# Kernel tuning notes

Measured on AMD Instinct MI355X. Metric: run time of the kernel, lower is better.

The kernel has to match this reference:

```python
import jax, jax.numpy as jnp
import numpy as np

B, N, C = 16, 4096, 91            # images, proposals/image, classes (incl. background)
H, W = 800.0, 1333.0              # image shape
SCORE_THRESH = 0.05
NMS_THRESH = 0.5
K = 100                           # detections_per_img (greedy NMS steps)
M = 4096                          # top-M candidate prefilter before NMS
OFFSET = 1.0e4                    # class offset for batched NMS (>> max coord)
DW_CLAMP = float(np.log(1000.0 / 16.0))


def setup_inputs():
    key = jax.random.key(0)
    k1, k2, k3, k4, k5, k6 = jax.random.split(key, 6)
    class_logits = jax.random.normal(k1, (B * N, C), jnp.float32) * 2.0
    box_regression = jax.random.normal(k2, (B * N, C * 4), jnp.float32) * 0.1
    # valid proposal boxes (x1 < x2, y1 < y2, inside image)
    x1 = jax.random.uniform(k3, (B, N, 1)) * (W - 64.0)
    y1 = jax.random.uniform(k4, (B, N, 1)) * (H - 64.0)
    bw = jax.random.uniform(k5, (B, N, 1)) * 256.0 + 16.0
    bh = jax.random.uniform(k6, (B, N, 1)) * 256.0 + 16.0
    proposals = jnp.concatenate([x1, y1, jnp.minimum(x1 + bw, W), jnp.minimum(y1 + bh, H)], -1)
    return {"class_logits": class_logits, "box_regression": box_regression, "proposals": proposals}


def _decode_and_clip(rel, props):
    w = props[..., 2] - props[..., 0]
    h = props[..., 3] - props[..., 1]
    cx = props[..., 0] + 0.5 * w
    cy = props[..., 1] + 0.5 * h
    dx = rel[..., 0] / 10.0
    dy = rel[..., 1] / 10.0
    dw = jnp.minimum(rel[..., 2] / 5.0, DW_CLAMP)
    dh = jnp.minimum(rel[..., 3] / 5.0, DW_CLAMP)
    pcx = dx * w[..., None] + cx[..., None]
    pcy = dy * h[..., None] + cy[..., None]
    pw = jnp.exp(dw) * w[..., None]
    ph = jnp.exp(dh) * h[..., None]
    boxes = jnp.stack([
        jnp.clip(pcx - 0.5 * pw, 0.0, W),
        jnp.clip(pcy - 0.5 * ph, 0.0, H),
        jnp.clip(pcx + 0.5 * pw, 0.0, W),
        jnp.clip(pcy + 0.5 * ph, 0.0, H)], -1)  # [B,N,C,4]
    return boxes


def _greedy_nms(boxes, scores):
    # boxes: [M,4] (already class-offset), scores: [M] (suppressed entries == -1)
    x1, y1, x2, y2 = boxes[:, 0], boxes[:, 1], boxes[:, 2], boxes[:, 3]
    area = (x2 - x1) * (y2 - y1)

    def step(sc, _):
        i = jnp.argmax(sc)
        s = sc[i]
        valid = s > 0.0
        iw = jnp.clip(jnp.minimum(x2, x2[i]) - jnp.maximum(x1, x1[i]), 0.0)
        ih = jnp.clip(jnp.minimum(y2, y2[i]) - jnp.maximum(y1, y1[i]), 0.0)
        inter = iw * ih
        iou = inter / (area + area[i] - inter + 1e-9)
        sc = jnp.where((iou > NMS_THRESH) & valid, -1.0, sc)
        sc = sc.at[i].set(-1.0)
        return sc, (i, s, valid)

    _, (idx, ss, vv) = jax.lax.scan(step, scores, None, length=K)
    return idx, ss, vv


def _post_image(boxes_all, scores_all):
    # boxes_all: [N,C,4] decoded+clipped, scores_all: [N,C] softmax scores
    boxes = boxes_all[:, 1:, :].reshape(-1, 4)          # drop background class 0
    scores = scores_all[:, 1:].reshape(-1)              # [N*(C-1)], class fastest
    labels = jnp.tile(jnp.arange(1, C, dtype=jnp.int32), N)
    scores = jnp.where(scores > SCORE_THRESH, scores, -1.0)
    top_s, top_i = jax.lax.top_k(scores, M)
    b = boxes[top_i]
    l = labels[top_i]
    ob = b + (l.astype(jnp.float32) * OFFSET)[:, None]  # batched_nms class-offset trick
    idx, ss, vv = _greedy_nms(ob, top_s)
    out_boxes = jnp.where(vv[:, None], b[idx], 0.0)     # [K,4]
    out_scores = jnp.where(vv, ss, 0.0)                 # [K]
    out_labels = jnp.where(vv, l[idx], -1)              # [K]
    return out_boxes, out_scores, out_labels, vv


def reference(class_logits, box_regression, proposals):
    pred_scores = jax.nn.softmax(class_logits, -1).reshape(B, N, C)
    rel = box_regression.reshape(B, N, C, 4)
    pred_boxes = _decode_and_clip(rel, proposals)
    boxes, scores, labels, valid = jax.vmap(_post_image)(pred_boxes, pred_scores)
    return boxes, scores, labels, valid
```

## Files before the change

kernel.cpp:

```cpp
#include <hip/hip_runtime.h>

typedef unsigned long long u64;
typedef unsigned int u32;

#define BDIM 16
#define NP   4096
#define NC   91
#define NCM1 90
#define MSEL 4096
#define NSORT 1024
#define KOUT 100
#define RSLOT 19
#define CAP_D (NP * RSLOT)
#define SCORE_T 0.05f
#define NMS_T   0.5f
#define OFFSETF 10000.0f
#define DW_CLAMP_F 4.135166556742356f
#define WF 1333.0f
#define HF 800.0f
#define GTMIN 384

#define TN 1024
#define RPB 64

#define DECODE_BODY(kvar, bvar, BOXDST, PACKDST)                                   \
    {                                                                              \
        int flat = (int)(~(u32)(kvar));                                            \
        int nidx = flat / NCM1;                                                    \
        int c    = flat - nidx * NCM1 + 1;                                         \
        const float* pr = props + ((long)(bvar) * NP + nidx) * 4;                  \
        float x1 = pr[0], y1 = pr[1], x2 = pr[2], y2 = pr[3];                      \
        float w = x2 - x1, h = y2 - y1;                                            \
        float cx = x1 + 0.5f * w, cy = y1 + 0.5f * h;                              \
        const float* rr = boxreg + (((long)(bvar) * NP + nidx) * NC + c) * 4;      \
        float dx = rr[0] / 10.0f, dy = rr[1] / 10.0f;                              \
        float dw = fminf(rr[2] / 5.0f, DW_CLAMP_F);                                \
        float dh = fminf(rr[3] / 5.0f, DW_CLAMP_F);                                \
        float pcx = __fadd_rn(__fmul_rn(dx, w), cx);                               \
        float pcy = __fadd_rn(__fmul_rn(dy, h), cy);                               \
        float pw  = __fmul_rn(expf(dw), w);                                        \
        float ph2 = __fmul_rn(expf(dh), h);                                        \
        float bx1 = fminf(fmaxf(pcx - 0.5f * pw, 0.0f), WF);                       \
        float by1 = fminf(fmaxf(pcy - 0.5f * ph2, 0.0f), HF);                      \
        float bx2 = fminf(fmaxf(pcx + 0.5f * pw, 0.0f), WF);                       \
        float by2 = fminf(fmaxf(pcy + 0.5f * ph2, 0.0f), HF);                      \
        BOXDST = make_float4(bx1, by1, bx2, by2);                                  \
        float offB = (float)c * OFFSETF;                                           \
        float ox1 = bx1 + offB, oy1 = by1 + offB;                                  \
        float ox2 = bx2 + offB, oy2 = by2 + offB;                                  \
        PACKDST = make_float2((ox2 - ox1) * (oy2 - oy1), (float)c);                \
    }

__global__ __launch_bounds__(64) void k_zero(int* __restrict__ gcount) {
    if (threadIdx.x < BDIM) gcount[threadIdx.x] = 0;
}

__global__ __launch_bounds__(256) void k_soft(const float* __restrict__ logits,
                                              u64* __restrict__ dense,
                                              int* __restrict__ gcount) {
    __shared__ u64 stage[RPB * RSLOT];
    __shared__ int s_cnt, s_base;

    int blk  = blockIdx.x;
    int b    = blk >> 6;
    int lane = threadIdx.x & 63;
    int wid  = threadIdx.x >> 6;

    if (threadIdx.x == 0) s_cnt = 0;
    __syncthreads();

    u64 lm = (1ull << lane) - 1ull;
    for (int it = 0; it < RPB / 4; ++it) {
        int row = blk * RPB + it * 4 + wid;
        const float* lg = logits + (long)row * NC;

        float v0 = lg[lane];
        float v1 = (lane < NC - 64) ? lg[64 + lane] : -3.0e38f;
        float mx = fmaxf(v0, v1);
#pragma unroll
        for (int s = 32; s; s >>= 1) mx = fmaxf(mx, __shfl_xor(mx, s));
        float e0 = expf(v0 - mx);
        float e1 = (lane < NC - 64) ? expf(v1 - mx) : 0.0f;
        float sum = e0 + e1;
#pragma unroll
        for (int s = 32; s; s >>= 1) sum += __shfl_xor(sum, s);

        float s0 = e0 / sum;
        float s1 = e1 / sum;

        int n = row & (NP - 1);
        bool p0 = (lane >= 1) && (s0 > SCORE_T);
        bool p1 = (lane < NC - 64) && (s1 > SCORE_T);
        u64 m0 = __ballot(p0);
        u64 m1 = __ballot(p1);
        int c0  = __popcll(m0);
        int cnt = c0 + __popcll(m1);

        int base = 0;
        if (lane == 0 && cnt) base = atomicAdd(&s_cnt, cnt);
        base = __shfl(base, 0);
        if (p0) {
            int pos  = base + __popcll(m0 & lm);
            int flat = n * NCM1 + (lane - 1);
            stage[pos] = ((u64)__float_as_uint(s0) << 32) | (u32)(~(u32)flat);
        }
        if (p1) {
            int pos  = base + c0 + __popcll(m1 & lm);
            int flat = n * NCM1 + (64 + lane - 1);
            stage[pos] = ((u64)__float_as_uint(s1) << 32) | (u32)(~(u32)flat);
        }
    }
    __syncthreads();

    if (threadIdx.x == 0) s_base = atomicAdd(&gcount[b], s_cnt);
    __syncthreads();
    int m = s_cnt, base = s_base;
    u64* kb = dense + (long)b * CAP_D + base;
    for (int i = threadIdx.x; i < m; i += 256) kb[i] = stage[i];
}

__device__ __forceinline__ u64 radix_rank(const u64* __restrict__ kb, int n, int rank,
                                          int* hist, int* p_sel, int* p_gt, int tid) {
    u64 prefix = 0, mask = 0;
    const int shifts[6] = {53, 42, 31, 20, 10, 0};
    const int bitsv [6] = {11, 11, 11, 11, 10, 10};

    for (int pass = 0; pass < 6; ++pass) {
        int shift = shifts[pass];
        int nb = 1 << bitsv[pass];
        if (tid < nb) hist[tid] = 0;
        if (tid + 1024 < nb) hist[tid + 1024] = 0;
        __syncthreads();
        for (int i = tid; i < n; i += 1024) {
            u64 k = kb[i];
            if ((k & mask) == prefix)
                atomicAdd(&hist[(int)((k >> shift) & (u64)(nb - 1))], 1);
        }
        __syncthreads();
        for (int d = 1; d < nb; d <<= 1) {
            int v0 = 0, v1 = 0;
            if (tid < nb && tid + d < nb) v0 = hist[tid + d];
            if (tid + 1024 < nb && tid + 1024 + d < nb) v1 = hist[tid + 1024 + d];
            __syncthreads();
            if (tid < nb) hist[tid] += v0;
            if (tid + 1024 < nb) hist[tid + 1024] += v1;
            __syncthreads();
        }
        for (int j = tid; j < nb; j += 1024) {
            int c  = hist[j];
            int cn = (j + 1 < nb) ? hist[j + 1] : 0;
            if (c >= rank && cn < rank) { *p_sel = j; *p_gt = cn; }
        }
        __syncthreads();
        prefix |= ((u64)(*p_sel)) << shift;
        mask   |= ((u64)(nb - 1)) << shift;
        rank   -= *p_gt;
        __syncthreads();
    }
    return prefix;
}

__device__ __forceinline__ u64 radix_upper(const u64* __restrict__ kb, int n, int rank,
                                           int* hist, int* p_sel, int* p_gt, int tid) {
    int rank0 = rank;
    u64 prefix = 0, mask = 0;
    const int shifts[6] = {53, 42, 31, 20, 10, 0};
    const int bitsv [6] = {11, 11, 11, 11, 10, 10};

    for (int pass = 0; pass < 6; ++pass) {
        int shift = shifts[pass];
        int nb = 1 << bitsv[pass];
        if (tid < nb) hist[tid] = 0;
        if (tid + 1024 < nb) hist[tid + 1024] = 0;
        __syncthreads();
        for (int i = tid; i < n; i += 1024) {
            u64 k = kb[i];
            if ((k & mask) == prefix)
                atomicAdd(&hist[(int)((k >> shift) & (u64)(nb - 1))], 1);
        }
        __syncthreads();
        for (int d = 1; d < nb; d <<= 1) {
            int v0 = 0, v1 = 0;
            if (tid < nb && tid + d < nb) v0 = hist[tid + d];
            if (tid + 1024 < nb && tid + 1024 + d < nb) v1 = hist[tid + 1024 + d];
            __syncthreads();
            if (tid < nb) hist[tid] += v0;
            if (tid + 1024 < nb) hist[tid + 1024] += v1;
            __syncthreads();
        }
        for (int j = tid; j < nb; j += 1024) {
            int c  = hist[j];
            int cn = (j + 1 < nb) ? hist[j + 1] : 0;
            if (c >= rank && cn < rank) { *p_sel = j; *p_gt = cn; }
        }
        __syncthreads();
        int sel = *p_sel, gt = *p_gt;
        rank -= gt;
        __syncthreads();
        if (pass < 5) {
            if (rank0 - rank >= GTMIN)
                return prefix + ((u64)(sel + 1) << shift);
            prefix |= ((u64)sel) << shift;
            mask   |= ((u64)(nb - 1)) << shift;
        } else {
            prefix |= ((u64)sel) << shift;
        }
    }
    return prefix;
}

__global__ __launch_bounds__(TN) void k_post(const u64* __restrict__ dense,
                                             const int* __restrict__ gcount,
                                             const float* __restrict__ boxreg,
                                             const float* __restrict__ props,
                                             float* __restrict__ out) {
    __shared__ __align__(16) char ldsbuf[131072];
    __shared__ int s_cnt, s_nacc, s_sel, s_gt;

    float4* sbox  = (float4*)ldsbuf;
    float2* spack = (float2*)(ldsbuf + 16384);
    u64*    skey  = (u64*)(ldsbuf + 24576);
    int*    hist  = (int*)(ldsbuf + 32768);

    int b = blockIdx.x, tid = threadIdx.x;
    int lane = tid & 63, wid = tid >> 6;
    int n = gcount[b]; if (n > CAP_D) n = CAP_D;
    const u64* kb = dense + (long)b * CAP_D;
    u64 lm = (1ull << lane) - 1ull;
    int npad = (n + TN - 1) & ~(TN - 1);

    u64 Bthr = 0ull;
    if (n > NSORT) Bthr = radix_upper(kb, n, NSORT, hist, &s_sel, &s_gt, tid);

    skey[tid] = 0ull;
    if (tid == 0) s_cnt = 0;
    __syncthreads();
    for (int i0 = tid; i0 < npad; i0 += TN) {
        bool inb = (i0 < n);
        u64 k = inb ? kb[i0] : 0ull;
        bool pred = inb && (k >= Bthr);
        u64 mb_ = __ballot(pred);
        int cnt = __popcll(mb_);
        int bp = 0;
        if (lane == 0 && cnt) bp = atomicAdd(&s_cnt, cnt);
        bp = __shfl(bp, 0);
        if (pred) {
            int pos = bp + __popcll(mb_ & lm);
            if (pos < NSORT) skey[pos] = k;
        }
    }
    __syncthreads();
    int mb = s_cnt; if (mb > NSORT) mb = NSORT;

    {
        u64 r = skey[tid];
        for (int kk = 2; kk <= NSORT; kk <<= 1) {
            for (int j = kk >> 1; j; j >>= 1) {
                u64 p;
                if (j >= 64) {
                    skey[tid] = r;
                    __syncthreads();
                    p = skey[tid ^ j];
                    __syncthreads();
                } else {
                    p = __shfl_xor(r, j);
                }
                bool lower = (tid & j) == 0;
                bool desc  = ((tid & kk) == 0);
                u64 mx = (r > p) ? r : p;
                u64 mn = (r > p) ? p : r;
                r = (lower == desc) ? mx : mn;
            }
        }
        skey[tid] = r;
        __syncthreads();
    }

    for (int i = tid; i < mb; i += TN) {
        u64 k = skey[i];
        float4 bx; float2 pk;
        DECODE_BODY(k, b, bx, pk);
        sbox[i] = bx;
        spack[i] = pk;
    }
    __syncthreads();

    float ax1_0 = 0, ay1_0 = 0, ax2_0 = 0, ay2_0 = 0, aar_0 = 0;
    float ax1_1 = 0, ay1_1 = 0, ax2_1 = 0, ay2_1 = 0, aar_1 = 0;
    int alb_0 = -1, alb_1 = -1;
    u64 aky_0 = 0, aky_1 = 0;
    int nacc = 0;

    if (wid == 0) {
        float4 Bv = sbox[0];
        float2 pk = spack[0];
        u64    ck = skey[0];
        for (int i = 0; i < mb && nacc < KOUT; ++i) {
            int ip = (i + 1 < mb) ? i + 1 : i;
            float4 nBv = sbox[ip];
            float2 npk = spack[ip];
            u64    nck = skey[ip];

            float areaB = pk.x;
            float labf  = pk.y;
            float off   = __fmul_rn(labf, OFFSETF);
            bool conf = false;
            if (lane < nacc && (float)alb_0 == labf) {
                float op1x = __fadd_rn(fminf(ax2_0, Bv.z), off);
                float op2x = __fadd_rn(fmaxf(ax1_0, Bv.x), off);
                float iw = fmaxf(op1x - op2x, 0.0f);
                float op1y = __fadd_rn(fminf(ay2_0, Bv.w), off);
                float op2y = __fadd_rn(fmaxf(ay1_0, Bv.y), off);
                float ih = fmaxf(op1y - op2y, 0.0f);
                float inter = iw * ih;
                float denom = areaB + aar_0 - inter + 1e-9f;
                if (inter / denom > NMS_T) conf = true;
            }
            if (64 + lane < nacc && (float)alb_1 == labf) {
                float op1x = __fadd_rn(fminf(ax2_1, Bv.z), off);
                float op2x = __fadd_rn(fmaxf(ax1_1, Bv.x), off);
                float iw = fmaxf(op1x - op2x, 0.0f);
                float op1y = __fadd_rn(fminf(ay2_1, Bv.w), off);
                float op2y = __fadd_rn(fmaxf(ay1_1, Bv.y), off);
                float ih = fmaxf(op1y - op2y, 0.0f);
                float inter = iw * ih;
                float denom = areaB + aar_1 - inter + 1e-9f;
                if (inter / denom > NMS_T) conf = true;
            }
            if (__ballot(conf) == 0ull) {
                if (nacc < 64) {
                    if (lane == nacc) {
                        ax1_0 = Bv.x; ay1_0 = Bv.y; ax2_0 = Bv.z; ay2_0 = Bv.w;
                        aar_0 = areaB; alb_0 = (int)labf; aky_0 = ck;
                    }
                } else {
                    if (lane == nacc - 64) {
                        ax1_1 = Bv.x; ay1_1 = Bv.y; ax2_1 = Bv.z; ay2_1 = Bv.w;
                        aar_1 = areaB; alb_1 = (int)labf; aky_1 = ck;
                    }
                }
                ++nacc;
            }
            Bv = nBv; pk = npk; ck = nck;
        }
        if (lane == 0) s_nacc = nacc;
    }
    __syncthreads();

    if (s_nacc < KOUT && Bthr != 0ull) {
        u64 T = 0ull;
        if (n > MSEL) T = radix_rank(kb, n, MSEL, hist, &s_sel, &s_gt, tid);

        u64*    fkey  = (u64*)ldsbuf;
        float4* fbox  = (float4*)(ldsbuf + 32768);
        float2* fpack = (float2*)(ldsbuf + 98304);

        for (int i = tid; i < MSEL; i += TN) fkey[i] = 0ull;
        if (tid == 0) s_cnt = 0;
        __syncthreads();
        for (int i0 = tid; i0 < npad; i0 += TN) {
            bool inb = (i0 < n);
            u64 k = inb ? kb[i0] : 0ull;
            bool pred = inb && (k >= T && k < Bthr);
            u64 mb_ = __ballot(pred);
            int cnt = __popcll(mb_);
            int bp = 0;
            if (lane == 0 && cnt) bp = atomicAdd(&s_cnt, cnt);
            bp = __shfl(bp, 0);
            if (pred) {
                int pos = bp + __popcll(mb_ & lm);
                if (pos < MSEL) fkey[pos] = k;
            }
        }
        __syncthreads();
        int mb2 = s_cnt; if (mb2 > MSEL) mb2 = MSEL;

        for (int kk = 2; kk <= MSEL; kk <<= 1) {
            for (int j = kk >> 1; j > 0; j >>= 1) {
                for (int t = tid; t < MSEL; t += TN) {
                    int l = t ^ j;
                    if (l > t) {
                        u64 a = fkey[t], c = fkey[l];
                        bool up = ((t & kk) == 0);
                        bool sw = up ? (a < c) : (a > c);
                        if (sw) { fkey[t] = c; fkey[l] = a; }
                    }
                }
                __syncthreads();
            }
        }

        for (int i = tid; i < mb2; i += TN) {
            u64 k = fkey[i];
            float4 bx; float2 pk;
            DECODE_BODY(k, b, bx, pk);
            fbox[i] = bx;
            fpack[i] = pk;
        }
        __syncthreads();

        if (wid == 0) {
            float4 Bv = fbox[0];
            float2 pk = fpack[0];
            u64    ck = fkey[0];
            for (int i = 0; i < mb2 && nacc < KOUT; ++i) {
                int ip = (i + 1 < mb2) ? i + 1 : i;
                float4 nBv = fbox[ip];
                float2 npk = fpack[ip];
                u64    nck = fkey[ip];

                float areaB = pk.x;
                float labf  = pk.y;
                float off   = __fmul_rn(labf, OFFSETF);
                bool conf = false;
                if (lane < nacc && (float)alb_0 == labf) {
                    float op1x = __fadd_rn(fminf(ax2_0, Bv.z), off);
                    float op2x = __fadd_rn(fmaxf(ax1_0, Bv.x), off);
                    float iw = fmaxf(op1x - op2x, 0.0f);
                    float op1y = __fadd_rn(fminf(ay2_0, Bv.w), off);
                    float op2y = __fadd_rn(fmaxf(ay1_0, Bv.y), off);
                    float ih = fmaxf(op1y - op2y, 0.0f);
                    float inter = iw * ih;
                    float denom = areaB + aar_0 - inter + 1e-9f;
                    if (inter / denom > NMS_T) conf = true;
                }
                if (64 + lane < nacc && (float)alb_1 == labf) {
                    float op1x = __fadd_rn(fminf(ax2_1, Bv.z), off);
                    float op2x = __fadd_rn(fmaxf(ax1_1, Bv.x), off);
                    float iw = fmaxf(op1x - op2x, 0.0f);
                    float op1y = __fadd_rn(fminf(ay2_1, Bv.w), off);
                    float op2y = __fadd_rn(fmaxf(ay1_1, Bv.y), off);
                    float ih = fmaxf(op1y - op2y, 0.0f);
                    float inter = iw * ih;
                    float denom = areaB + aar_1 - inter + 1e-9f;
                    if (inter / denom > NMS_T) conf = true;
                }
                if (__ballot(conf) == 0ull) {
                    if (nacc < 64) {
                        if (lane == nacc) {
                            ax1_0 = Bv.x; ay1_0 = Bv.y; ax2_0 = Bv.z; ay2_0 = Bv.w;
                            aar_0 = areaB; alb_0 = (int)labf; aky_0 = ck;
                        }
                    } else {
                        if (lane == nacc - 64) {
                            ax1_1 = Bv.x; ay1_1 = Bv.y; ax2_1 = Bv.z; ay2_1 = Bv.w;
                            aar_1 = areaB; alb_1 = (int)labf; aky_1 = ck;
                        }
                    }
                    ++nacc;
                }
                Bv = nBv; pk = npk; ck = nck;
            }
            if (lane == 0) s_nacc = nacc;
        }
        __syncthreads();
    }

    int na = s_nacc; if (na > KOUT) na = KOUT;
    if (wid == 0) {
        if (lane < na) {
            int a = lane;
            float* ob = out + ((long)b * KOUT + a) * 4;
            ob[0] = ax1_0; ob[1] = ay1_0; ob[2] = ax2_0; ob[3] = ay2_0;
            out[BDIM * KOUT * 4 + b * KOUT + a] = __uint_as_float((u32)(aky_0 >> 32));
            out[BDIM * KOUT * 5 + b * KOUT + a] = (float)alb_0;
            out[BDIM * KOUT * 6 + b * KOUT + a] = 1.0f;
        }
        if (64 + lane < na) {
            int a = 64 + lane;
            float* ob = out + ((long)b * KOUT + a) * 4;
            ob[0] = ax1_1; ob[1] = ay1_1; ob[2] = ax2_1; ob[3] = ay2_1;
            out[BDIM * KOUT * 4 + b * KOUT + a] = __uint_as_float((u32)(aky_1 >> 32));
            out[BDIM * KOUT * 5 + b * KOUT + a] = (float)alb_1;
            out[BDIM * KOUT * 6 + b * KOUT + a] = 1.0f;
        }
    }
    for (int a = tid; a < KOUT; a += TN) {
        if (a >= na) {
            float* ob = out + ((long)b * KOUT + a) * 4;
            ob[0] = 0.0f; ob[1] = 0.0f; ob[2] = 0.0f; ob[3] = 0.0f;
            out[BDIM * KOUT * 4 + b * KOUT + a] = 0.0f;
            out[BDIM * KOUT * 5 + b * KOUT + a] = -1.0f;
            out[BDIM * KOUT * 6 + b * KOUT + a] = 0.0f;
        }
    }
}

extern "C" void kernel_launch(void* const* d_in, const int* in_sizes, int n_in,
                              void* d_out, int out_size, void* d_ws, size_t ws_size,
                              hipStream_t stream) {
    const float* logits = (const float*)d_in[0];
    const float* boxreg = (const float*)d_in[1];
    const float* props  = (const float*)d_in[2];
    float* out = (float*)d_out;

    char* ws = (char*)d_ws;
    int* gcount = (int*)(ws + 0);
    u64* dense  = (u64*)(ws + 1024);

    k_zero<<<1, 64, 0, stream>>>(gcount);
    k_soft<<<(BDIM * NP) / RPB, 256, 0, stream>>>(logits, dense, gcount);
    k_post<<<BDIM, TN, 0, stream>>>(dense, gcount, boxreg, props, out);
}
```

Baseline: 84.18 us.

## Build top-bits histogram and hot-key list in softmax kernel to skip radix passes

The softmax kernel now builds a per-image 2048-bin histogram over the top 11 key bits and also writes a compact list of high-score candidates (score >= 0.25). The post kernel prefix-sums that histogram to find the top-1024 threshold bin directly, so it can usually skip the multi-pass radix select over the dense candidate array. When the threshold lies in the hot range, it compacts from the small hot list instead of rescanning all dense keys. This removes repeated global scans from the single-block-per-image post kernel. In exchange it adds shared atomics and global histogram atomics to k_soft, a larger zeroing kernel, and fallback paths for when the estimate overflows.

```diff
diff --git a/kernel.cpp b/kernel.cpp
--- a/kernel.cpp
+++ b/kernel.cpp
@@ -19,6 +19,8 @@
 #define WF 1333.0f
 #define HF 800.0f
 #define GTMIN 384
+#define HCAP 4096
+#define FKEY (((u64)0x3E800000u) << 32)
 
 #define TN 1024
 #define RPB 64
@@ -51,22 +53,37 @@
         PACKDST = make_float2((ox2 - ox1) * (oy2 - oy1), (float)c);                \
     }
 
-__global__ __launch_bounds__(64) void k_zero(int* __restrict__ gcount) {
-    if (threadIdx.x < BDIM) gcount[threadIdx.x] = 0;
+__global__ __launch_bounds__(1024) void k_zero(int* __restrict__ gcount,
+                                               int* __restrict__ hcnt,
+                                               int* __restrict__ ghist) {
+    int blk = blockIdx.x;
+    if (blk == 0) {
+        if (threadIdx.x < BDIM) gcount[threadIdx.x] = 0;
+        if (threadIdx.x >= 64 && threadIdx.x < 64 + BDIM) hcnt[threadIdx.x - 64] = 0;
+    } else {
+        int* g = ghist + (blk - 1) * 2048;
+        for (int i = threadIdx.x; i < 2048; i += 1024) g[i] = 0;
+    }
 }
 
 __global__ __launch_bounds__(256) void k_soft(const float* __restrict__ logits,
                                               u64* __restrict__ dense,
-                                              int* __restrict__ gcount) {
+                                              int* __restrict__ gcount,
+                                              u64* __restrict__ hot,
+                                              int* __restrict__ hcnt,
+                                              int* __restrict__ ghist) {
     __shared__ u64 stage[RPB * RSLOT];
-    __shared__ int s_cnt, s_base;
+    __shared__ u64 hstage[256];
+    __shared__ int lhist[2048];
+    __shared__ int s_cnt, s_base, s_hcnt, s_hbase;
 
     int blk  = blockIdx.x;
     int b    = blk >> 6;
     int lane = threadIdx.x & 63;
     int wid  = threadIdx.x >> 6;
 
-    if (threadIdx.x == 0) s_cnt = 0;
+    if (threadIdx.x == 0) { s_cnt = 0; s_hcnt = 0; }
+    for (int i = threadIdx.x; i < 2048; i += 256) lhist[i] = 0;
     __syncthreads();
 
     u64 lm = (1ull << lane) - 1ull;
@@ -91,6 +108,8 @@
         int n = row & (NP - 1);
         bool p0 = (lane >= 1) && (s0 > SCORE_T);
         bool p1 = (lane < NC - 64) && (s1 > SCORE_T);
+        u64 key0 = ((u64)__float_as_uint(s0) << 32) | (u32)(~(u32)(n * NCM1 + (lane - 1)));
+        u64 key1 = ((u64)__float_as_uint(s1) << 32) | (u32)(~(u32)(n * NCM1 + (64 + lane - 1)));
         u64 m0 = __ballot(p0);
         u64 m1 = __ballot(p1);
         int c0  = __popcll(m0);
@@ -100,23 +119,46 @@
         if (lane == 0 && cnt) base = atomicAdd(&s_cnt, cnt);
         base = __shfl(base, 0);
         if (p0) {
-            int pos  = base + __popcll(m0 & lm);
-            int flat = n * NCM1 + (lane - 1);
-            stage[pos] = ((u64)__float_as_uint(s0) << 32) | (u32)(~(u32)flat);
+            stage[base + __popcll(m0 & lm)] = key0;
+            atomicAdd(&lhist[(int)(key0 >> 53)], 1);
         }
         if (p1) {
-            int pos  = base + c0 + __popcll(m1 & lm);
-            int flat = n * NCM1 + (64 + lane - 1);
-            stage[pos] = ((u64)__float_as_uint(s1) << 32) | (u32)(~(u32)flat);
-        }
+            stage[base + c0 + __popcll(m1 & lm)] = key1;
+            atomicAdd(&lhist[(int)(key1 >> 53)], 1);
+        }
+
+        bool q0 = p0 && (s0 >= 0.25f);
+        bool q1 = p1 && (s1 >= 0.25f);
+        u64 h0 = __ballot(q0);
+        u64 h1 = __ballot(q1);
+        int hc0 = __popcll(h0);
+        int hrow = hc0 + __popcll(h1);
+        int hb = 0;
+        if (lane == 0 && hrow) hb = atomicAdd(&s_hcnt, hrow);
+        hb = __shfl(hb, 0);
+        if (q0) hstage[hb + __popcll(h0 & lm)] = key0;
+        if (q1) hstage[hb + hc0 + __popcll(h1 & lm)] = key1;
     }
     __syncthreads();
 
-    if (threadIdx.x == 0) s_base = atomicAdd(&gcount[b], s_cnt);
+    if (threadIdx.x == 0) {
+        s_base  = atomicAdd(&gcount[b], s_cnt);
+        s_hbase = atomicAdd(&hcnt[b], s_hcnt);
+    }
     __syncthreads();
     int m = s_cnt, base = s_base;
     u64* kb = dense + (long)b * CAP_D + base;
     for (int i = threadIdx.x; i < m; i += 256) kb[i] = stage[i];
+    int hm = s_hcnt, hb2 = s_hbase;
+    u64* hbp = hot + (long)b * HCAP;
+    for (int i = threadIdx.x; i < hm; i += 256) {
+        int pos = hb2 + i;
+        if (pos < HCAP) hbp[pos] = hstage[i];
+    }
+    for (int i = threadIdx.x; i < 2048; i += 256) {
+        int v = lhist[i];
+        if (v) atomicAdd(&ghist[b * 2048 + i], v);
+    }
 }
 
 __device__ __forceinline__ u64 radix_rank(const u64* __restrict__ kb, int n, int rank,
@@ -211,6 +253,9 @@
 
 __global__ __launch_bounds__(TN) void k_post(const u64* __restrict__ dense,
                                              const int* __restrict__ gcount,
+                                             const u64* __restrict__ hot,
+                                             const int* __restrict__ hcnt,
+                                             const int* __restrict__ ghist,
                                              const float* __restrict__ boxreg,
                                              const float* __restrict__ props,
                                              float* __restrict__ out) {
@@ -230,26 +275,91 @@
     int npad = (n + TN - 1) & ~(TN - 1);
 
     u64 Bthr = 0ull;
-    if (n > NSORT) Bthr = radix_upper(kb, n, NSORT, hist, &s_sel, &s_gt, tid);
+    bool hist_ok = false;
+    if (n > NSORT) {
+        for (int i = tid; i < 2048; i += TN) hist[i] = ghist[b * 2048 + i];
+        __syncthreads();
+        for (int d = 1; d < 2048; d <<= 1) {
+            int v0 = 0, v1 = 0;
+            if (tid + d < 2048) v0 = hist[tid + d];
+            if (tid + 1024 + d < 2048) v1 = hist[tid + 1024 + d];
+            __syncthreads();
+            hist[tid] += v0;
+            if (tid + 1024 + d < 2048 || tid + 1024 < 2048) hist[tid + 1024] += v1;
+            __syncthreads();
+        }
+        for (int j = tid; j < 2048; j += TN) {
+            int c  = hist[j];
+            int cn = (j + 1 < 2048) ? hist[j + 1] : 0;
+            if (c >= NSORT && cn < NSORT) { s_sel = j; s_gt = cn; }
+        }
+        __syncthreads();
+        int sel = s_sel, gt = s_gt;
+        __syncthreads();
+        if (gt >= GTMIN) { Bthr = ((u64)(sel + 1)) << 53; hist_ok = true; }
+        else             Bthr = radix_upper(kb, n, NSORT, hist, &s_sel, &s_gt, tid);
+    }
+    int hn = hcnt[b];
+    bool use_hot = hist_ok && (Bthr >= FKEY) && (hn <= HCAP);
 
     skey[tid] = 0ull;
     if (tid == 0) s_cnt = 0;
     __syncthreads();
-    for (int i0 = tid; i0 < npad; i0 += TN) {
-        bool inb = (i0 < n);
-        u64 k = inb ? kb[i0] : 0ull;
-        bool pred = inb && (k >= Bthr);
-        u64 mb_ = __ballot(pred);
-        int cnt = __popcll(mb_);
-        int bp = 0;
-        if (lane == 0 && cnt) bp = atomicAdd(&s_cnt, cnt);
-        bp = __shfl(bp, 0);
-        if (pred) {
-            int pos = bp + __popcll(mb_ & lm);
-            if (pos < NSORT) skey[pos] = k;
+    if (use_hot) {
+        const u64* hb = hot + (long)b * HCAP;
+        int hpad = (hn + TN - 1) & ~(TN - 1);
+        for (int i0 = tid; i0 < hpad; i0 += TN) {
+            bool inb = (i0 < hn);
+            u64 k = inb ? hb[i0] : 0ull;
+            bool pred = inb && (k >= Bthr);
+            u64 mb_ = __ballot(pred);
+            int cnt = __popcll(mb_);
+            int bp = 0;
+            if (lane == 0 && cnt) bp = atomicAdd(&s_cnt, cnt);
+            bp = __shfl(bp, 0);
+            if (pred) {
+                int pos = bp + __popcll(mb_ & lm);
+                if (pos < NSORT) skey[pos] = k;
+            }
+        }
+    } else {
+        for (int i0 = tid; i0 < npad; i0 += TN) {
+            bool inb = (i0 < n);
+            u64 k = inb ? kb[i0] : 0ull;
+            bool pred = inb && (k >= Bthr);
+            u64 mb_ = __ballot(pred);
+            int cnt = __popcll(mb_);
+            int bp = 0;
+            if (lane == 0 && cnt) bp = atomicAdd(&s_cnt, cnt);
+            bp = __shfl(bp, 0);
+            if (pred) {
+                int pos = bp + __popcll(mb_ & lm);
+                if (pos < NSORT) skey[pos] = k;
+            }
         }
     }
     __syncthreads();
+    if (s_cnt > NSORT) {
+        Bthr = radix_upper(kb, n, NSORT, hist, &s_sel, &s_gt, tid);
+        skey[tid] = 0ull;
+        if (tid == 0) s_cnt = 0;
+        __syncthreads();
+        for (int i0 = tid; i0 < npad; i0 += TN) {
+            bool inb = (i0 < n);
+            u64 k = inb ? kb[i0] : 0ull;
+            bool pred = inb && (k >= Bthr);
+            u64 mb_ = __ballot(pred);
+            int cnt = __popcll(mb_);
+            int bp = 0;
+            if (lane == 0 && cnt) bp = atomicAdd(&s_cnt, cnt);
+            bp = __shfl(bp, 0);
+            if (pred) {
+                int pos = bp + __popcll(mb_ & lm);
+                if (pos < NSORT) skey[pos] = k;
+            }
+        }
+        __syncthreads();
+    }
     int mb = s_cnt; if (mb > NSORT) mb = NSORT;
 
     {
@@ -496,9 +606,12 @@
 
     char* ws = (char*)d_ws;
     int* gcount = (int*)(ws + 0);
-    u64* dense  = (u64*)(ws + 1024);
-
-    k_zero<<<1, 64, 0, stream>>>(gcount);
-    k_soft<<<(BDIM * NP) / RPB, 256, 0, stream>>>(logits, dense, gcount);
-    k_post<<<BDIM, TN, 0, stream>>>(dense, gcount, boxreg, props, out);
+    int* hcnt   = (int*)(ws + 256);
+    int* ghist  = (int*)(ws + 1024);
+    u64* hot    = (u64*)(ws + 132096);
+    u64* dense  = (u64*)(ws + 1048576);
+
+    k_zero<<<17, 1024, 0, stream>>>(gcount, hcnt, ghist);
+    k_soft<<<(BDIM * NP) / RPB, 256, 0, stream>>>(logits, dense, gcount, hot, hcnt, ghist);
+    k_post<<<BDIM, TN, 0, stream>>>(dense, gcount, hot, hcnt, ghist, boxreg, props, out);
 }
```

Measured after the change: 78.55 us. 6.7% less time.
